# Kernel optimization log

Measured on AMD Instinct MI355X. Metric: run time of the kernel, lower is better.

The kernel has to match this reference:

```python
import jax, jax.numpy as jnp
import numpy as np

B, T, H = 512, 256, 256


def setup_inputs() -> dict:
    key = jax.random.key(0)
    ks = jax.random.split(key, 12)
    s = 1.0 / np.sqrt(H)
    return {
        "h_tilde": jax.random.normal(ks[0], (B, H), jnp.float32),
        "c_t": jax.random.normal(ks[1], (B, H), jnp.float32),
        "h_history": jax.random.normal(ks[2], (B, T, H), jnp.float32),
        "deltaT_hist": jax.random.uniform(ks[3], (B, T, 1), jnp.float32),
        "deltaL_hist": jax.random.uniform(ks[4], (B, T, 1), jnp.float32),
        "W_I": jax.random.normal(ks[5], (H, 2 * H), jnp.float32) * s,
        "W_Ih": jax.random.normal(ks[6], (H, H), jnp.float32) * s,
        "W_I1T": jax.random.normal(ks[7], (H, 1), jnp.float32),
        "W_I1L": jax.random.normal(ks[8], (H, 1), jnp.float32),
        "b_I": jnp.zeros((H,), jnp.float32),
        "W_oI": jax.random.normal(ks[9], (H, H), jnp.float32) * s,
        "b_oI": jnp.zeros((H,), jnp.float32),
        "v_t": jax.random.normal(ks[10], (H,), jnp.float32),
    }


def reference(h_tilde, c_t, h_history, deltaT_hist, deltaL_hist,
              W_I, W_Ih, W_I1T, W_I1L, b_I, W_oI, b_oI, v_t):
    # h_hat: [B, 2H]; current projection: [B, H]
    h_hat = jnp.concatenate([h_tilde, c_t], axis=1)
    current_proj = h_hat @ W_I.T
    # Batched per-step additive attention pre-activation I_ti: [B, T, H]
    I = (current_proj[:, None, :]
         + jnp.einsum('bth,oh->bto', h_history, W_Ih)
         + deltaT_hist * W_I1T[:, 0]          # [B,T,1]*[H] -> [B,T,H]
         + deltaL_hist * W_I1L[:, 0]
         + b_I)
    o = jnp.tanh(jnp.einsum('bti,oi->bto', I, W_oI) + b_oI)  # [B, T, H]
    scores = jnp.einsum('bth,h->bt', o, v_t)                  # [B, T]
    alpha = jax.nn.softmax(scores, axis=1)
    s_t = jnp.einsum('bt,bth->bh', alpha, h_history)          # [B, H]
    return (s_t, alpha)
```

## Files before the change

kernel.cpp:

```cpp
#include <hip/hip_runtime.h>
#include <hip/hip_bf16.h>
#include <hip/hip_fp16.h>

#define Hdim 256
#define Tdim 256
#define Bdim 512
#define TT   64
#define NTILE (Tdim / TT)
#define NTHR 256

typedef __attribute__((ext_vector_type(8))) short s16x8;
typedef __attribute__((ext_vector_type(8))) _Float16 f16x8;
typedef __attribute__((ext_vector_type(2))) _Float16 f16x2;
typedef __attribute__((ext_vector_type(4))) float f32x4;
typedef unsigned short u16;
typedef unsigned int u32;

__device__ __forceinline__ u32 cvt_pk_f16(float lo, float hi) {
    auto v = __builtin_amdgcn_cvt_pkrtz(lo, hi);
    return __builtin_bit_cast(u32, v);
}
__device__ __forceinline__ u16 f2h_rne(float x) {
    _Float16 h = (_Float16)x;
    return __builtin_bit_cast(u16, h);
}
__device__ __forceinline__ f32x4 mfma16h(s16x8 a, s16x8 b, f32x4 c) {
    return __builtin_amdgcn_mfma_f32_16x16x32_f16(
        __builtin_bit_cast(f16x8, a), __builtin_bit_cast(f16x8, b), c, 0, 0, 0);
}
__device__ __forceinline__ float fast_tanh(float z) {
    float e = __expf(2.0f * z);
    return 1.0f - 2.0f * __builtin_amdgcn_rcpf(e + 1.0f);
}
__device__ __forceinline__ s16x8 bfrag_f32(const float* __restrict__ wp) {
    float4 x0 = *(const float4*)(wp + 0);
    float4 x1 = *(const float4*)(wp + 4);
    uint4 uu = make_uint4(cvt_pk_f16(x0.x, x0.y), cvt_pk_f16(x0.z, x0.w),
                          cvt_pk_f16(x1.x, x1.y), cvt_pk_f16(x1.z, x1.w));
    return __builtin_bit_cast(s16x8, uu);
}

__global__ __launch_bounds__(256) void prep_kernel(
        const float* __restrict__ W_Ih, const float* __restrict__ W_oI,
        const float* __restrict__ W_I1T, const float* __restrict__ W_I1L,
        const float* __restrict__ h_tilde, const float* __restrict__ c_t,
        const float* __restrict__ W_I, const float* __restrict__ b_I,
        const float* __restrict__ b_oI,
        u16* __restrict__ Wph, float* __restrict__ wT2, float* __restrict__ wL2,
        float* __restrict__ cp2) {
    __shared__ char smem[98304];
    __shared__ float redT[4], redL[4];
    const int tid = threadIdx.x;
    const int w = tid >> 6, lane = tid & 63;
    const int c = lane & 15, g = lane >> 4;

    if (blockIdx.x < Hdim) {
        float* sWo = (float*)smem;
        const int o = blockIdx.x;
        const int j = tid;
        sWo[j] = W_oI[o * Hdim + j];
        __syncthreads();
        float a0 = 0.f, a1 = 0.f, a2 = 0.f, a3 = 0.f;
        #pragma unroll 8
        for (int i = 0; i < Hdim; i += 4) {
            a0 += sWo[i + 0] * W_Ih[(i + 0) * Hdim + j];
            a1 += sWo[i + 1] * W_Ih[(i + 1) * Hdim + j];
            a2 += sWo[i + 2] * W_Ih[(i + 2) * Hdim + j];
            a3 += sWo[i + 3] * W_Ih[(i + 3) * Hdim + j];
        }
        const float acc = (a0 + a1) + (a2 + a3);
        const int dst = (o >> 4) * 4096 + (j >> 5) * 512 + ((j >> 3) & 3) * 128
                      + (o & 15) * 8 + (j & 7);
        Wph[dst] = f2h_rne(acc);
        float pT = sWo[j] * W_I1T[j];
        float pL = sWo[j] * W_I1L[j];
        #pragma unroll
        for (int d = 1; d < 64; d <<= 1) {
            pT += __shfl_xor(pT, d, 64);
            pL += __shfl_xor(pL, d, 64);
        }
        if (lane == 0) { redT[w] = pT; redL[w] = pL; }
        __syncthreads();
        if (j == 0) {
            wT2[o] = redT[0] + redT[1] + redT[2] + redT[3];
            wL2[o] = redL[0] + redL[1] + redL[2] + redL[3];
        }
    } else {
        char* hh_b  = smem;
        char* cpl_b = smem + 65536;
        const int b0 = (blockIdx.x - Hdim) * 64;
        const u32 swzA = (u32)((c & 7) << 4);
        const f32x4 fz = {0.f, 0.f, 0.f, 0.f};
        {
            const int srow = tid >> 2;
            const int sj = tid & 3;
            const u32 sbb = (u32)(srow * 1024);
            const u32 ssz = (u32)((srow & 7) << 4);
            #pragma unroll
            for (int ch = 0; ch < 8; ++ch) {
                const int col = ch * 64 + sj * 16;
                const float* src = (col < Hdim)
                    ? (h_tilde + (size_t)(b0 + srow) * Hdim + col)
                    : (c_t + (size_t)(b0 + srow) * Hdim + col - Hdim);
                float4 f0 = *(const float4*)(src + 0);
                float4 f1 = *(const float4*)(src + 4);
                float4 f2 = *(const float4*)(src + 8);
                float4 f3 = *(const float4*)(src + 12);
                uint4 ua = make_uint4(cvt_pk_f16(f0.x, f0.y), cvt_pk_f16(f0.z, f0.w),
                                      cvt_pk_f16(f1.x, f1.y), cvt_pk_f16(f1.z, f1.w));
                uint4 ub = make_uint4(cvt_pk_f16(f2.x, f2.y), cvt_pk_f16(f2.z, f2.w),
                                      cvt_pk_f16(f3.x, f3.y), cvt_pk_f16(f3.z, f3.w));
                *(uint4*)(hh_b + ((sbb + (u32)(col * 2) + 0) ^ ssz)) = ua;
                *(uint4*)(hh_b + ((sbb + (u32)(col * 2) + 16) ^ ssz)) = ub;
            }
        }
        __syncthreads();
        f32x4 acc[4][4];
        #pragma unroll
        for (int m = 0; m < 4; ++m)
            #pragma unroll
            for (int n = 0; n < 4; ++n) acc[m][n] = fz;
        #pragma unroll
        for (int ks = 0; ks < 16; ++ks) {
            s16x8 a[4];
            #pragma unroll
            for (int m = 0; m < 4; ++m)
                a[m] = *(const s16x8*)(hh_b +
                    (((u32)((m * 16 + c) * 1024 + ks * 64 + g * 16)) ^ swzA));
            #pragma unroll
            for (int n = 0; n < 4; ++n) {
                const int o = w * 64 + n * 16 + c;
                const s16x8 bf = bfrag_f32(W_I + (size_t)o * (2 * Hdim) + ks * 32 + g * 8);
                #pragma unroll
                for (int m = 0; m < 4; ++m) acc[m][n] = mfma16h(a[m], bf, acc[m][n]);
            }
        }
        #pragma unroll
        for (int n = 0; n < 4; ++n) {
            const int o = w * 64 + n * 16 + c;
            const float bi = b_I[o];
            const u32 ocol2 = (u32)((o & ~1) * 2);
            #pragma unroll
            for (int m = 0; m < 4; ++m) {
                #pragma unroll
                for (int r = 0; r < 4; ++r) {
                    const int row = m * 16 + g * 4 + r;
                    float z = acc[m][n][r] + bi;
                    float zsw = __shfl_xor(z, 1, 64);
                    if (!(c & 1)) {
                        u32 h2 = cvt_pk_f16(z, zsw);
                        *(u32*)(cpl_b + (((u32)(row * 512) + ocol2) ^ ((u32)((row & 7) << 4)))) = h2;
                    }
                }
            }
        }
        __syncthreads();
        f32x4 acc2[4][4];
        #pragma unroll
        for (int m = 0; m < 4; ++m)
            #pragma unroll
            for (int n = 0; n < 4; ++n) acc2[m][n] = fz;
        #pragma unroll
        for (int ks = 0; ks < 8; ++ks) {
            s16x8 a[4];
            #pragma unroll
            for (int m = 0; m < 4; ++m)
                a[m] = *(const s16x8*)(cpl_b +
                    (((u32)((m * 16 + c) * 512 + ks * 64 + g * 16)) ^ swzA));
            #pragma unroll
            for (int n = 0; n < 4; ++n) {
                const int o = w * 64 + n * 16 + c;
                const s16x8 bf = bfrag_f32(W_oI + (size_t)o * Hdim + ks * 32 + g * 8);
                #pragma unroll
                for (int m = 0; m < 4; ++m) acc2[m][n] = mfma16h(a[m], bf, acc2[m][n]);
            }
        }
        #pragma unroll
        for (int n = 0; n < 4; ++n) {
            const int o = w * 64 + n * 16 + c;
            const float bo = b_oI[o];
            #pragma unroll
            for (int m = 0; m < 4; ++m)
                #pragma unroll
                for (int r = 0; r < 4; ++r)
                    cp2[(size_t)(b0 + m * 16 + g * 4 + r) * Hdim + o] = acc2[m][n][r] + bo;
        }
    }
}

__global__ __launch_bounds__(NTHR, 4) void scores_kernel(
        const float* __restrict__ hist, const float* __restrict__ dT,
        const float* __restrict__ dL, const float* __restrict__ cp2,
        const u16* __restrict__ Wph,
        const float* __restrict__ wT2, const float* __restrict__ wL2,
        const float* __restrict__ v_t, float* __restrict__ scores,
        float* __restrict__ Spart, float* __restrict__ mpart,
        float* __restrict__ lpart) {
    __shared__ u16 lds_u[TT * Hdim];
    __shared__ float dtl[TT], dll[TT];
    __shared__ float sc_part[4][TT];
    __shared__ float p_sh[TT];
    __shared__ float ml_sh[2];
    __shared__ float sacc2[2][Hdim];

    const int bid = blockIdx.x;
    const int b = bid >> 2;
    const int t0 = (bid & 3) * TT;
    const int tid = threadIdx.x;
    const int w = tid >> 6, lane = tid & 63;
    const int c = lane & 15, g = lane >> 4;
    const int ob = w * 64;

    const int wfrag = lane * 8;
    #define WOFF(n, ks) ((w * 4 + (n)) * 4096 + (ks) * 512 + wfrag)

    if (tid < TT) {
        dtl[tid] = dT[b * Tdim + t0 + tid];
        dll[tid] = dL[b * Tdim + t0 + tid];
    }

    {
        const int srow = tid >> 2;
        const int sj = tid & 3;
        const float* srcb = hist + ((size_t)b * Tdim + t0 + srow) * Hdim;
        const u32 sbb = (u32)(srow * 512);
        const u32 ssz = (u32)((srow & 7) << 4);
        char* dst = (char*)lds_u;
        #pragma unroll
        for (int ch = 0; ch < 4; ++ch) {
            const int col = ch * 64 + sj * 16;
            float4 f0 = *(const float4*)(srcb + col + 0);
            float4 f1 = *(const float4*)(srcb + col + 4);
            float4 f2 = *(const float4*)(srcb + col + 8);
            float4 f3 = *(const float4*)(srcb + col + 12);
            uint4 ua = make_uint4(cvt_pk_f16(f0.x, f0.y), cvt_pk_f16(f0.z, f0.w),
                                  cvt_pk_f16(f1.x, f1.y), cvt_pk_f16(f1.z, f1.w));
            uint4 ub = make_uint4(cvt_pk_f16(f2.x, f2.y), cvt_pk_f16(f2.z, f2.w),
                                  cvt_pk_f16(f3.x, f3.y), cvt_pk_f16(f3.z, f3.w));
            *(uint4*)(dst + ((sbb + (u32)(col * 2) + 0) ^ ssz)) = ua;
            *(uint4*)(dst + ((sbb + (u32)(col * 2) + 16) ^ ssz)) = ub;
        }
    }
    __syncthreads();

    const f32x4 fz = {0.f, 0.f, 0.f, 0.f};
    const u32 swzA = (u32)((c & 7) << 4);

    f32x4 acc[4][4];
    #pragma unroll
    for (int m = 0; m < 4; ++m)
        #pragma unroll
        for (int n = 0; n < 4; ++n) acc[m][n] = fz;
    {
        const char* hb = (const char*)lds_u;
        #pragma unroll
        for (int ks = 0; ks < 8; ++ks) {
            s16x8 a[4];
            #pragma unroll
            for (int m = 0; m < 4; ++m)
                a[m] = *(const s16x8*)(hb +
                    (((u32)((m * 16 + c) * 512 + g * 16 + ks * 64)) ^ swzA));
            #pragma unroll
            for (int n = 0; n < 4; ++n) {
                const s16x8 bh = *(const s16x8*)(Wph + WOFF(n, ks));
                #pragma unroll
                for (int m = 0; m < 4; ++m)
                    acc[m][n] = mfma16h(a[m], bh, acc[m][n]);
            }
        }
    }

    float cpv[4], wtv[4], wlv[4], vvv[4];
    #pragma unroll
    for (int n = 0; n < 4; ++n) {
        const int o = ob + n * 16 + c;
        cpv[n] = cp2[(size_t)b * Hdim + o];
        wtv[n] = wT2[o];
        wlv[n] = wL2[o];
        vvv[n] = v_t[o];
    }
    #pragma unroll
    for (int m = 0; m < 4; ++m) {
        #pragma unroll
        for (int r = 0; r < 4; ++r) {
            const int row = m * 16 + g * 4 + r;
            const float dtr = dtl[row], dlr = dll[row];
            float s = 0.f;
            #pragma unroll
            for (int n = 0; n < 4; ++n) {
                float z = acc[m][n][r] + cpv[n] + dtr * wtv[n] + dlr * wlv[n];
                s += fast_tanh(z) * vvv[n];
            }
            s += __shfl_xor(s, 1, 64);
            s += __shfl_xor(s, 2, 64);
            s += __shfl_xor(s, 4, 64);
            s += __shfl_xor(s, 8, 64);
            if (c == 0) sc_part[w][row] = s;
        }
    }
    __syncthreads();

    if (tid < TT) {
        float s = sc_part[0][tid] + sc_part[1][tid] + sc_part[2][tid] + sc_part[3][tid];
        scores[b * Tdim + t0 + tid] = s;
        float mx = s;
        #pragma unroll
        for (int d = 1; d < 64; d <<= 1) mx = fmaxf(mx, __shfl_xor(mx, d, 64));
        float p = __expf(s - mx);
        float l = p;
        #pragma unroll
        for (int d = 1; d < 64; d <<= 1) l += __shfl_xor(l, d, 64);
        p_sh[tid] = p;
        if (tid == 0) { ml_sh[0] = mx; ml_sh[1] = l; }
    }
    __syncthreads();

    {
        const int half = tid >> 7;
        const int pp = tid & 127;
        const char* hb = (const char*)lds_u;
        float s0 = 0.f, s1 = 0.f;
        #pragma unroll 8
        for (int i = 0; i < 32; ++i) {
            const int t = half * 32 + i;
            const float pv = p_sh[t];
            const u32 hw = *(const u32*)(hb + (((u32)(t * 512 + pp * 4)) ^ ((u32)((t & 7) << 4))));
            const f16x2 hv = __builtin_bit_cast(f16x2, hw);
            s0 += pv * (float)hv[0];
            s1 += pv * (float)hv[1];
        }
        sacc2[half][2 * pp] = s0;
        sacc2[half][2 * pp + 1] = s1;
    }
    __syncthreads();
    Spart[(size_t)bid * Hdim + tid] = sacc2[0][tid] + sacc2[1][tid];
    if (tid == 0) { mpart[bid] = ml_sh[0]; lpart[bid] = ml_sh[1]; }
    #undef WOFF
}

__global__ __launch_bounds__(256) void combine_kernel(
        const float* __restrict__ Spart, const float* __restrict__ mpart,
        const float* __restrict__ lpart, float* __restrict__ out) {
    const int b = blockIdx.x;
    const int tid = threadIdx.x;
    __shared__ float fsh[4], inv_l_sh, m_sh;
    if (tid == 0) {
        const float m0 = mpart[4 * b + 0], m1 = mpart[4 * b + 1];
        const float m2 = mpart[4 * b + 2], m3 = mpart[4 * b + 3];
        const float m = fmaxf(fmaxf(m0, m1), fmaxf(m2, m3));
        const float f0 = __expf(m0 - m), f1 = __expf(m1 - m);
        const float f2 = __expf(m2 - m), f3 = __expf(m3 - m);
        const float l = f0 * lpart[4 * b + 0] + f1 * lpart[4 * b + 1]
                      + f2 * lpart[4 * b + 2] + f3 * lpart[4 * b + 3];
        fsh[0] = f0; fsh[1] = f1; fsh[2] = f2; fsh[3] = f3;
        inv_l_sh = 1.0f / l;
        m_sh = m;
    }
    __syncthreads();
    const float inv_l = inv_l_sh;
    const float S = fsh[0] * Spart[(size_t)(4 * b + 0) * Hdim + tid]
                  + fsh[1] * Spart[(size_t)(4 * b + 1) * Hdim + tid]
                  + fsh[2] * Spart[(size_t)(4 * b + 2) * Hdim + tid]
                  + fsh[3] * Spart[(size_t)(4 * b + 3) * Hdim + tid];
    out[b * Hdim + tid] = S * inv_l;
    float* scores = out + Bdim * Hdim;
    const float sc = scores[b * Tdim + tid];
    scores[b * Tdim + tid] = __expf(sc - m_sh) * inv_l;
}

extern "C" void kernel_launch(void* const* d_in, const int* in_sizes, int n_in,
                              void* d_out, int out_size, void* d_ws, size_t ws_size,
                              hipStream_t stream) {
    const float* h_tilde = (const float*)d_in[0];
    const float* c_t     = (const float*)d_in[1];
    const float* hist    = (const float*)d_in[2];
    const float* dT      = (const float*)d_in[3];
    const float* dL      = (const float*)d_in[4];
    const float* W_I     = (const float*)d_in[5];
    const float* W_Ih    = (const float*)d_in[6];
    const float* W_I1T   = (const float*)d_in[7];
    const float* W_I1L   = (const float*)d_in[8];
    const float* b_I     = (const float*)d_in[9];
    const float* W_oI    = (const float*)d_in[10];
    const float* b_oI    = (const float*)d_in[11];
    const float* v_t     = (const float*)d_in[12];
    float* out = (float*)d_out;

    char* ws = (char*)d_ws;
    u16* Wph     = (u16*)ws;
    float* cp2   = (float*)(ws + 131072);
    float* wT2   = (float*)(ws + 655360);
    float* wL2   = (float*)(ws + 656384);
    float* Spart = (float*)(ws + 657408);
    float* mpart = (float*)(ws + 657408 + 2097152);
    float* lpart = (float*)(ws + 657408 + 2105344);
    float* scores = out + Bdim * Hdim;

    prep_kernel<<<dim3(Hdim + 8), dim3(256), 0, stream>>>(
        W_Ih, W_oI, W_I1T, W_I1L, h_tilde, c_t, W_I, b_I, b_oI,
        Wph, wT2, wL2, cp2);
    scores_kernel<<<dim3(Bdim * NTILE), dim3(NTHR), 0, stream>>>(
        hist, dT, dL, cp2, Wph, wT2, wL2, v_t, scores, Spart, mpart, lpart);
    combine_kernel<<<dim3(Bdim), dim3(256), 0, stream>>>(Spart, mpart, lpart, out);
}
```

Measured before the change: 98.71 us.

## Fuse softmax combine into scores kernel via last-block counter; widen prep grid

Removes the separate combine kernel launch. The last of the four tile blocks per batch row, found with an atomic counter and threadfence, now merges the partial max, sum and weighted-sum results and normalizes the scores in place. The prep kernel's projection GEMM is also split into 16-row blocks instead of 64-row blocks, so 32 blocks share that work and each uses less shared memory. This adds atomics and fences to every scores block, and each prep block reloads W_I and W_oI, raising redundant weight traffic.

After: 336.7 us. +241.1%, slower.

```diff
diff --git a/kernel.cpp b/kernel.cpp
--- a/kernel.cpp
+++ b/kernel.cpp
@@ -8,6 +8,7 @@
 #define TT   64
 #define NTILE (Tdim / TT)
 #define NTHR 256
+#define NCP  32
 
 typedef __attribute__((ext_vector_type(8))) short s16x8;
 typedef __attribute__((ext_vector_type(8))) _Float16 f16x8;
@@ -47,12 +48,14 @@
         const float* __restrict__ W_I, const float* __restrict__ b_I,
         const float* __restrict__ b_oI,
         u16* __restrict__ Wph, float* __restrict__ wT2, float* __restrict__ wL2,
-        float* __restrict__ cp2) {
-    __shared__ char smem[98304];
+        float* __restrict__ cp2, int* __restrict__ cnt) {
+    __shared__ char smem[24576];
     __shared__ float redT[4], redL[4];
     const int tid = threadIdx.x;
     const int w = tid >> 6, lane = tid & 63;
     const int c = lane & 15, g = lane >> 4;
+
+    if (blockIdx.x < 2) cnt[blockIdx.x * 256 + tid] = 0;
 
     if (blockIdx.x < Hdim) {
         float* sWo = (float*)smem;
@@ -87,18 +90,19 @@
         }
     } else {
         char* hh_b  = smem;
-        char* cpl_b = smem + 65536;
-        const int b0 = (blockIdx.x - Hdim) * 64;
+        char* cpl_b = smem + 16384;
+        const int b0 = (blockIdx.x - Hdim) * 16;
         const u32 swzA = (u32)((c & 7) << 4);
         const f32x4 fz = {0.f, 0.f, 0.f, 0.f};
+
         {
-            const int srow = tid >> 2;
-            const int sj = tid & 3;
+            const int srow = tid >> 4;
+            const int sj = tid & 15;
             const u32 sbb = (u32)(srow * 1024);
             const u32 ssz = (u32)((srow & 7) << 4);
             #pragma unroll
-            for (int ch = 0; ch < 8; ++ch) {
-                const int col = ch * 64 + sj * 16;
+            for (int ch = 0; ch < 2; ++ch) {
+                const int col = sj * 32 + ch * 16;
                 const float* src = (col < Hdim)
                     ? (h_tilde + (size_t)(b0 + srow) * Hdim + col)
                     : (c_t + (size_t)(b0 + srow) * Hdim + col - Hdim);
@@ -115,24 +119,19 @@
             }
         }
         __syncthreads();
-        f32x4 acc[4][4];
-        #pragma unroll
-        for (int m = 0; m < 4; ++m)
-            #pragma unroll
-            for (int n = 0; n < 4; ++n) acc[m][n] = fz;
+
+        f32x4 acc[4];
+        #pragma unroll
+        for (int n = 0; n < 4; ++n) acc[n] = fz;
         #pragma unroll
         for (int ks = 0; ks < 16; ++ks) {
-            s16x8 a[4];
-            #pragma unroll
-            for (int m = 0; m < 4; ++m)
-                a[m] = *(const s16x8*)(hh_b +
-                    (((u32)((m * 16 + c) * 1024 + ks * 64 + g * 16)) ^ swzA));
+            const s16x8 a = *(const s16x8*)(hh_b +
+                (((u32)(c * 1024 + ks * 64 + g * 16)) ^ swzA));
             #pragma unroll
             for (int n = 0; n < 4; ++n) {
                 const int o = w * 64 + n * 16 + c;
                 const s16x8 bf = bfrag_f32(W_I + (size_t)o * (2 * Hdim) + ks * 32 + g * 8);
-                #pragma unroll
-                for (int m = 0; m < 4; ++m) acc[m][n] = mfma16h(a[m], bf, acc[m][n]);
+                acc[n] = mfma16h(a, bf, acc[n]);
             }
         }
         #pragma unroll
@@ -141,38 +140,30 @@
             const float bi = b_I[o];
             const u32 ocol2 = (u32)((o & ~1) * 2);
             #pragma unroll
-            for (int m = 0; m < 4; ++m) {
-                #pragma unroll
-                for (int r = 0; r < 4; ++r) {
-                    const int row = m * 16 + g * 4 + r;
-                    float z = acc[m][n][r] + bi;
-                    float zsw = __shfl_xor(z, 1, 64);
-                    if (!(c & 1)) {
-                        u32 h2 = cvt_pk_f16(z, zsw);
-                        *(u32*)(cpl_b + (((u32)(row * 512) + ocol2) ^ ((u32)((row & 7) << 4)))) = h2;
-                    }
+            for (int r = 0; r < 4; ++r) {
+                const int row = g * 4 + r;
+                float z = acc[n][r] + bi;
+                float zsw = __shfl_xor(z, 1, 64);
+                if (!(c & 1)) {
+                    u32 h2 = cvt_pk_f16(z, zsw);
+                    *(u32*)(cpl_b + (((u32)(row * 512) + ocol2) ^ ((u32)((row & 7) << 4)))) = h2;
                 }
             }
         }
         __syncthreads();
-        f32x4 acc2[4][4];
-        #pragma unroll
-        for (int m = 0; m < 4; ++m)
-            #pragma unroll
-            for (int n = 0; n < 4; ++n) acc2[m][n] = fz;
+
+        f32x4 acc2[4];
+        #pragma unroll
+        for (int n = 0; n < 4; ++n) acc2[n] = fz;
         #pragma unroll
         for (int ks = 0; ks < 8; ++ks) {
-            s16x8 a[4];
-            #pragma unroll
-            for (int m = 0; m < 4; ++m)
-                a[m] = *(const s16x8*)(cpl_b +
-                    (((u32)((m * 16 + c) * 512 + ks * 64 + g * 16)) ^ swzA));
+            const s16x8 a = *(const s16x8*)(cpl_b +
+                (((u32)(c * 512 + ks * 64 + g * 16)) ^ swzA));
             #pragma unroll
             for (int n = 0; n < 4; ++n) {
                 const int o = w * 64 + n * 16 + c;
                 const s16x8 bf = bfrag_f32(W_oI + (size_t)o * Hdim + ks * 32 + g * 8);
-                #pragma unroll
-                for (int m = 0; m < 4; ++m) acc2[m][n] = mfma16h(a[m], bf, acc2[m][n]);
+                acc2[n] = mfma16h(a, bf, acc2[n]);
             }
         }
         #pragma unroll
@@ -180,10 +171,8 @@
             const int o = w * 64 + n * 16 + c;
             const float bo = b_oI[o];
             #pragma unroll
-            for (int m = 0; m < 4; ++m)
-                #pragma unroll
-                for (int r = 0; r < 4; ++r)
-                    cp2[(size_t)(b0 + m * 16 + g * 4 + r) * Hdim + o] = acc2[m][n][r] + bo;
+            for (int r = 0; r < 4; ++r)
+                cp2[(size_t)(b0 + g * 4 + r) * Hdim + o] = acc2[n][r] + bo;
         }
     }
 }
@@ -193,16 +182,19 @@
         const float* __restrict__ dL, const float* __restrict__ cp2,
         const u16* __restrict__ Wph,
         const float* __restrict__ wT2, const float* __restrict__ wL2,
-        const float* __restrict__ v_t, float* __restrict__ scores,
+        const float* __restrict__ v_t, float* __restrict__ out,
         float* __restrict__ Spart, float* __restrict__ mpart,
-        float* __restrict__ lpart) {
+        float* __restrict__ lpart, int* __restrict__ cnt) {
     __shared__ u16 lds_u[TT * Hdim];
     __shared__ float dtl[TT], dll[TT];
     __shared__ float sc_part[4][TT];
     __shared__ float p_sh[TT];
     __shared__ float ml_sh[2];
     __shared__ float sacc2[2][Hdim];
-
+    __shared__ int amlast;
+    __shared__ float fsh2[4], invl_sh, msh;
+
+    float* scores = out + Bdim * Hdim;
     const int bid = blockIdx.x;
     const int b = bid >> 2;
     const int t0 = (bid & 3) * TT;
@@ -335,37 +327,35 @@
     __syncthreads();
     Spart[(size_t)bid * Hdim + tid] = sacc2[0][tid] + sacc2[1][tid];
     if (tid == 0) { mpart[bid] = ml_sh[0]; lpart[bid] = ml_sh[1]; }
+
+    __threadfence();
+    if (tid == 0) amlast = (atomicAdd(&cnt[b], 1) == NTILE - 1) ? 1 : 0;
+    __syncthreads();
+    if (amlast) {
+        __threadfence();
+        if (tid == 0) {
+            const float m0 = mpart[4 * b + 0], m1 = mpart[4 * b + 1];
+            const float m2 = mpart[4 * b + 2], m3 = mpart[4 * b + 3];
+            const float m = fmaxf(fmaxf(m0, m1), fmaxf(m2, m3));
+            const float f0 = __expf(m0 - m), f1 = __expf(m1 - m);
+            const float f2 = __expf(m2 - m), f3 = __expf(m3 - m);
+            const float l = f0 * lpart[4 * b + 0] + f1 * lpart[4 * b + 1]
+                          + f2 * lpart[4 * b + 2] + f3 * lpart[4 * b + 3];
+            fsh2[0] = f0; fsh2[1] = f1; fsh2[2] = f2; fsh2[3] = f3;
+            invl_sh = 1.0f / l;
+            msh = m;
+        }
+        __syncthreads();
+        const float inv_l = invl_sh;
+        const float S = fsh2[0] * Spart[(size_t)(4 * b + 0) * Hdim + tid]
+                      + fsh2[1] * Spart[(size_t)(4 * b + 1) * Hdim + tid]
+                      + fsh2[2] * Spart[(size_t)(4 * b + 2) * Hdim + tid]
+                      + fsh2[3] * Spart[(size_t)(4 * b + 3) * Hdim + tid];
+        out[b * Hdim + tid] = S * inv_l;
+        const float sc = scores[b * Tdim + tid];
+        scores[b * Tdim + tid] = __expf(sc - msh) * inv_l;
+    }
     #undef WOFF
-}
-
-__global__ __launch_bounds__(256) void combine_kernel(
-        const float* __restrict__ Spart, const float* __restrict__ mpart,
-        const float* __restrict__ lpart, float* __restrict__ out) {
-    const int b = blockIdx.x;
-    const int tid = threadIdx.x;
-    __shared__ float fsh[4], inv_l_sh, m_sh;
-    if (tid == 0) {
-        const float m0 = mpart[4 * b + 0], m1 = mpart[4 * b + 1];
-        const float m2 = mpart[4 * b + 2], m3 = mpart[4 * b + 3];
-        const float m = fmaxf(fmaxf(m0, m1), fmaxf(m2, m3));
-        const float f0 = __expf(m0 - m), f1 = __expf(m1 - m);
-        const float f2 = __expf(m2 - m), f3 = __expf(m3 - m);
-        const float l = f0 * lpart[4 * b + 0] + f1 * lpart[4 * b + 1]
-                      + f2 * lpart[4 * b + 2] + f3 * lpart[4 * b + 3];
-        fsh[0] = f0; fsh[1] = f1; fsh[2] = f2; fsh[3] = f3;
-        inv_l_sh = 1.0f / l;
-        m_sh = m;
-    }
-    __syncthreads();
-    const float inv_l = inv_l_sh;
-    const float S = fsh[0] * Spart[(size_t)(4 * b + 0) * Hdim + tid]
-                  + fsh[1] * Spart[(size_t)(4 * b + 1) * Hdim + tid]
-                  + fsh[2] * Spart[(size_t)(4 * b + 2) * Hdim + tid]
-                  + fsh[3] * Spart[(size_t)(4 * b + 3) * Hdim + tid];
-    out[b * Hdim + tid] = S * inv_l;
-    float* scores = out + Bdim * Hdim;
-    const float sc = scores[b * Tdim + tid];
-    scores[b * Tdim + tid] = __expf(sc - m_sh) * inv_l;
 }
 
 extern "C" void kernel_launch(void* const* d_in, const int* in_sizes, int n_in,
@@ -394,12 +384,11 @@
     float* Spart = (float*)(ws + 657408);
     float* mpart = (float*)(ws + 657408 + 2097152);
     float* lpart = (float*)(ws + 657408 + 2105344);
-    float* scores = out + Bdim * Hdim;
-
-    prep_kernel<<<dim3(Hdim + 8), dim3(256), 0, stream>>>(
+    int*   cnt   = (int*)(ws + 657408 + 2113536);
+
+    prep_kernel<<<dim3(Hdim + NCP), dim3(256), 0, stream>>>(
         W_Ih, W_oI, W_I1T, W_I1L, h_tilde, c_t, W_I, b_I, b_oI,
-        Wph, wT2, wL2, cp2);
+        Wph, wT2, wL2, cp2, cnt);
     scores_kernel<<<dim3(Bdim * NTILE), dim3(NTHR), 0, stream>>>(
-        hist, dT, dL, cp2, Wph, wT2, wL2, v_t, scores, Spart, mpart, lpart);
-    combine_kernel<<<dim3(Bdim), dim3(256), 0, stream>>>(Spart, mpart, lpart, out);
-}
+        hist, dT, dL, cp2, Wph, wT2, wL2, v_t, out, Spart, mpart, lpart, cnt);
+}
```
